# Performance work log

Hardware: AMD Instinct MI355X
Metric: run time of the kernel (lower is better)

Reference implementation:

```python
import jax, jax.numpy as jnp
import numpy as np

N_ITER = 3


def squash(v):
    # v: [..., out_C]; scale by ||v||^2/(1+||v||^2) and normalize by ||v||
    sq = jnp.sum(v * v, axis=-1, keepdims=True)
    return (sq / (1.0 + sq)) * v / jnp.sqrt(sq)


def setup_inputs() -> dict:
    key = jax.random.key(0)
    k1, k2 = jax.random.split(key)
    B, n_nodes, n_caps, in_C, out_C = 64, 2048, 32, 16, 32
    x = jax.random.normal(k1, (B, n_nodes, in_C), dtype=jnp.float32)
    route_weights = 0.1 * jax.random.normal(k2, (n_nodes, n_caps, in_C, out_C), dtype=jnp.float32)
    return {"x": x, "route_weights": route_weights}


def reference(x, route_weights):
    # priors: [B, n_nodes, n_caps, out_C]
    priors = jnp.einsum('bni,nkio->bnko', x, route_weights)
    logits = jnp.zeros_like(priors)
    outputs = None
    for i in range(N_ITER):
        probs = jax.nn.softmax(logits, axis=2)            # over n_caps
        s = jnp.sum(probs * priors, axis=1, keepdims=True)  # [B,1,n_caps,out_C]
        outputs = squash(s)
        if i != N_ITER - 1:
            delta = jnp.sum(priors * outputs, axis=-1, keepdims=True)
            logits = logits + delta
    return outputs
```

## Files before the change

### kernel.cpp

```cpp
#include <hip/hip_runtime.h>
#include <math.h>


#define BATCH 64
#define NN    2048
#define NK    32
#define NI    16
#define NO    32

#define PNB   16
#define NSETS (NN / PNB)
#define NCH   4
#define XT_JS 528

typedef __bf16 bf16x8 __attribute__((ext_vector_type(8)));
typedef float  f32x16 __attribute__((ext_vector_type(16)));

__device__ __forceinline__ unsigned short f2bf(float f) {
    unsigned int x = __float_as_uint(f);
    unsigned int lsb = (x >> 16) & 1u;
    x += 0x7fffu + lsb;
    return (unsigned short)(x >> 16);
}
__device__ __forceinline__ float bflo(unsigned int u) { return __uint_as_float(u << 16); }
__device__ __forceinline__ float bfhi(unsigned int u) { return __uint_as_float(u & 0xffff0000u); }

__global__ __launch_bounds__(256) void wqt_kernel(const float* __restrict__ Wg,
                                                  unsigned short* __restrict__ wq) {
    const int w    = threadIdx.x >> 6;
    const int lane = threadIdx.x & 63;
    const int task = blockIdx.x * 4 + w;
    const int o  = lane & 31;
    const int ih = lane >> 5;
    const float* src = Wg + (size_t)task * (NI * NO);
    unsigned short d[8];
#pragma unroll
    for (int j = 0; j < 8; ++j)
        d[j] = f2bf(src[(ih * 8 + j) * NO + o]);
    *(uint4*)(wq + (size_t)task * (NO * NI) + o * NI + ih * 8) = *(uint4*)d;
}

template <int PASS>
__global__ __launch_bounds__(1024) void fused_pass(
    const float* __restrict__ xg,
    const unsigned short* __restrict__ wq,
    const float* __restrict__ vpart,
    float* __restrict__ logits0,
    float* __restrict__ part)
{
    __shared__ unsigned short xt_lds[PNB * XT_JS];
    __shared__ float delta_lds[2][32 * 33];

    const int tid  = threadIdx.x;
    const int w    = tid >> 6;
    const int lane = tid & 63;
    const int l5   = lane & 31;
    const int h5   = lane >> 5;
    const int set  = blockIdx.x;
    const int hb   = blockIdx.y;
    const int k0   = 2 * w, k1 = 2 * w + 1;
    const int gb5  = hb * 32 + l5;
    const int sb   = tid >> 5;
    const int sk   = tid & 31;
    const int nbase = set * PNB;

#pragma unroll
    for (int rr = 0; rr < 2; ++rr) {
        const int id  = tid + rr * 1024;
        const int bl  = id >> 6;
        const int rem = id & 63;
        const int j   = rem >> 2;
        const int i4  = rem & 3;
        float4 v = *(const float4*)(xg + ((size_t)(hb * 32 + bl) * NN + (nbase + j)) * NI + i4 * 4);
        ushort4 o4;
        o4.x = f2bf(v.x); o4.y = f2bf(v.y); o4.z = f2bf(v.z); o4.w = f2bf(v.w);
        *(ushort4*)(xt_lds + j * XT_JS + bl * 16 + i4 * 4) = o4;
    }
    __syncthreads();

    unsigned orp0[8], orp1[8];
    if constexpr (PASS >= 1) {
        float v0[16], v1[16];
        float sq0 = 0.f, sq1 = 0.f;
#pragma unroll
        for (int r = 0; r < 16; ++r) {
            const int o = (r & 3) + 8 * (r >> 2) + 4 * h5;
            float a = 0.f, b = 0.f;
#pragma unroll
            for (int c = 0; c < NCH; ++c) {
                a += vpart[(((size_t)c * NK + k0) * NO + o) * BATCH + gb5];
                b += vpart[(((size_t)c * NK + k1) * NO + o) * BATCH + gb5];
            }
            v0[r] = a; v1[r] = b;
            sq0 = fmaf(a, a, sq0);
            sq1 = fmaf(b, b, sq1);
        }
        sq0 += __shfl_xor(sq0, 32);
        sq1 += __shfl_xor(sq1, 32);
        const float cf0 = sq0 / ((1.f + sq0) * sqrtf(sq0));
        const float cf1 = sq1 / ((1.f + sq1) * sqrtf(sq1));
#pragma unroll
        for (int q = 0; q < 8; ++q) {
            orp0[q] = (unsigned)f2bf(v0[2 * q] * cf0) | ((unsigned)f2bf(v0[2 * q + 1] * cf0) << 16);
            orp1[q] = (unsigned)f2bf(v1[2 * q] * cf1) | ((unsigned)f2bf(v1[2 * q + 1] * cf1) << 16);
        }
    }

    float sa0[16], sa1[16];
#pragma unroll
    for (int r = 0; r < 16; ++r) { sa0[r] = 0.f; sa1[r] = 0.f; }

    bf16x8 b0N, b1N;
    float gN = 0.f;
    {
        const int n = nbase;
        b0N = *(const bf16x8*)(wq + (size_t)n * (NK * NO * NI) + k0 * (NO * NI) + l5 * NI + h5 * 8);
        b1N = *(const bf16x8*)(wq + (size_t)n * (NK * NO * NI) + k1 * (NO * NI) + l5 * NI + h5 * 8);
        if constexpr (PASS == 2)
            gN = logits0[(size_t)n * (BATCH * NK) + hb * 1024 + tid];
    }

    int buf = 0;
    for (int j = 0; j < PNB; ++j) {
        const int n = nbase + j;
        const bf16x8 b0C = b0N, b1C = b1N;
        const float gC = gN;
        if (j < PNB - 1) {
            const int n2 = n + 1;
            b0N = *(const bf16x8*)(wq + (size_t)n2 * (NK * NO * NI) + k0 * (NO * NI) + l5 * NI + h5 * 8);
            b1N = *(const bf16x8*)(wq + (size_t)n2 * (NK * NO * NI) + k1 * (NO * NI) + l5 * NI + h5 * 8);
            if constexpr (PASS == 2)
                gN = logits0[(size_t)n2 * (BATCH * NK) + hb * 1024 + tid];
        }
        const bf16x8 aC = *(const bf16x8*)(xt_lds + j * XT_JS + l5 * 16 + h5 * 8);

        f32x16 c0, c1;
#pragma unroll
        for (int r = 0; r < 16; ++r) { c0[r] = 0.f; c1[r] = 0.f; }
        c0 = __builtin_amdgcn_mfma_f32_32x32x16_bf16(b0C, aC, c0, 0, 0, 0);
        c1 = __builtin_amdgcn_mfma_f32_32x32x16_bf16(b1C, aC, c1, 0, 0, 0);

        if constexpr (PASS == 0) {
#pragma unroll
            for (int r = 0; r < 16; ++r) { sa0[r] += c0[r]; sa1[r] += c1[r]; }
        } else {
            float d0 = 0.f, d1 = 0.f;
#pragma unroll
            for (int r = 0; r < 16; ++r) {
                const unsigned u0 = orp0[r >> 1], u1 = orp1[r >> 1];
                const float o0 = (r & 1) ? bfhi(u0) : bflo(u0);
                const float o1 = (r & 1) ? bfhi(u1) : bflo(u1);
                d0 = fmaf(c0[r], o0, d0);
                d1 = fmaf(c1[r], o1, d1);
            }
            d0 += __shfl_xor(d0, 32);
            d1 += __shfl_xor(d1, 32);

            delta_lds[buf][l5 * 33 + (h5 ? k1 : k0)] = h5 ? d1 : d0;
            __syncthreads();

            float l = delta_lds[buf][sb * 33 + sk];
            if constexpr (PASS == 1)
                logits0[(size_t)n * (BATCH * NK) + hb * 1024 + tid] = l;
            else
                l += gC;
            float e = __expf(l);
            float s = e;
#pragma unroll
            for (int mask = 1; mask < 32; mask <<= 1)
                s += __shfl_xor(s, mask);
            delta_lds[buf][sb * 33 + sk] = e / s;
            __syncthreads();

            const float p0 = delta_lds[buf][l5 * 33 + k0];
            const float p1 = delta_lds[buf][l5 * 33 + k1];
#pragma unroll
            for (int r = 0; r < 16; ++r) {
                sa0[r] = fmaf(p0, c0[r], sa0[r]);
                sa1[r] = fmaf(p1, c1[r], sa1[r]);
            }
            buf ^= 1;
        }
    }

    const float scale = (PASS == 0) ? (1.f / NK) : 1.f;
    float* pb = part + ((size_t)(hb * NSETS + set) << 15);
#pragma unroll
    for (int r = 0; r < 16; ++r) {
        const int o = (r & 3) + 8 * (r >> 2) + 4 * h5;
        pb[(k0 * NO + o) * 32 + l5] = sa0[r] * scale;
        pb[(k1 * NO + o) * 32 + l5] = sa1[r] * scale;
    }
}

__global__ __launch_bounds__(1024) void reduce_stageA(
    const float* __restrict__ part,
    float* __restrict__ vpart)
{
    const int k  = blockIdx.x;
    const int hb = blockIdx.y;
    const int c  = blockIdx.z;
    const int t  = threadIdx.x;
    const int o  = t >> 5;
    const int b  = t & 31;

    const float* src = part + ((size_t)(hb * NSETS + c * (NSETS / NCH)) << 15)
                            + (k << 10) + (o << 5) + b;
    float v0 = 0.f, v1 = 0.f, v2 = 0.f, v3 = 0.f;
#pragma unroll 4
    for (int s = 0; s < NSETS / NCH; s += 4) {
        v0 += src[(size_t)(s + 0) << 15];
        v1 += src[(size_t)(s + 1) << 15];
        v2 += src[(size_t)(s + 2) << 15];
        v3 += src[(size_t)(s + 3) << 15];
    }
    vpart[(((size_t)c * NK + k) * NO + o) * BATCH + hb * 32 + b] = (v0 + v1) + (v2 + v3);
}

__global__ __launch_bounds__(1024) void reduce_final(
    const float* __restrict__ vpart,
    float* __restrict__ outp)
{
    __shared__ float s_lds[32 * 33];
    __shared__ float cf_lds[32];
    const int k  = blockIdx.x;
    const int hb = blockIdx.y;
    const int t  = threadIdx.x;
    const int o  = t >> 5;
    const int b  = t & 31;

    float v = 0.f;
#pragma unroll
    for (int c = 0; c < NCH; ++c)
        v += vpart[(((size_t)c * NK + k) * NO + o) * BATCH + hb * 32 + b];
    s_lds[o * 33 + b] = v;
    __syncthreads();
    if (t < 32) {
        float sq = 0.f;
#pragma unroll
        for (int oo = 0; oo < 32; ++oo) { const float x = s_lds[oo * 33 + t]; sq = fmaf(x, x, sq); }
        cf_lds[t] = sq / ((1.f + sq) * sqrtf(sq));
    }
    __syncthreads();
    const int bq = t >> 5, oq = t & 31;
    outp[(size_t)(hb * 32 + bq) * 1024 + k * 32 + oq] = s_lds[oq * 33 + bq] * cf_lds[bq];
}


#define LBB 32
#define LNCHUNK 8
#define LNBLK (NN / LNCHUNK)
#define LTHREADS 512
#define WK_STRIDE 516

template <int PASS>
__global__ __launch_bounds__(LTHREADS, 1) void legacy_pass(
    const float* __restrict__ xg, const float* __restrict__ Wg,
    const float* __restrict__ outvL, float* __restrict__ logits,
    float* __restrict__ partial)
{
    __shared__ float w_lds[NK * WK_STRIDE];
    __shared__ float x_lds[LBB][NI + 1];
    __shared__ float delta_lds[LBB][NK + 1];
    const int t = threadIdx.x, nb = blockIdx.x, bg = blockIdx.y;
    const int b0 = bg * LBB;
    const int k = t >> 4, bq = t & 15, bl0 = bq * 2, bl1 = bq * 2 + 1;
    float acc0[NO], acc1[NO];
#pragma unroll
    for (int o = 0; o < NO; ++o) { acc0[o] = 0.f; acc1[o] = 0.f; }
    float outr0[NO], outr1[NO];
    if constexpr (PASS >= 1) {
        const float4* o0 = (const float4*)&outvL[((b0 + bl0) * NK + k) * NO];
        const float4* o1 = (const float4*)&outvL[((b0 + bl1) * NK + k) * NO];
#pragma unroll
        for (int q = 0; q < NO / 4; ++q) {
            float4 a = o0[q]; float4 b = o1[q];
            outr0[4*q+0]=a.x; outr0[4*q+1]=a.y; outr0[4*q+2]=a.z; outr0[4*q+3]=a.w;
            outr1[4*q+0]=b.x; outr1[4*q+1]=b.y; outr1[4*q+2]=b.z; outr1[4*q+3]=b.w;
        }
    }
    for (int j = 0; j < LNCHUNK; ++j) {
        const int n = nb * LNCHUNK + j;
        __syncthreads();
        {
            const float4* src = (const float4*)(Wg + (size_t)n * (NK * NI * NO));
#pragma unroll
            for (int r = 0; r < (NK * NI * NO / 4) / LTHREADS; ++r) {
                int idx4 = t + r * LTHREADS;
                float4 v = src[idx4];
                int e = idx4 * 4, kk = e >> 9, rem = e & 511;
                *(float4*)&w_lds[kk * WK_STRIDE + rem] = v;
            }
        }
        { int bl = t >> 4, i = t & 15;
          x_lds[bl][i] = xg[((size_t)(b0 + bl) * NN + n) * NI + i]; }
        __syncthreads();
        if constexpr (PASS == 0) {
#pragma unroll
            for (int i = 0; i < NI; ++i) {
                float xa = x_lds[bl0][i], xb = x_lds[bl1][i];
                const float* wrow = &w_lds[k * WK_STRIDE + i * NO];
#pragma unroll
                for (int o = 0; o < NO; ++o) {
                    float w = wrow[o];
                    acc0[o] = fmaf(xa, w, acc0[o]);
                    acc1[o] = fmaf(xb, w, acc1[o]);
                }
            }
        } else {
            float pr0[NO], pr1[NO];
#pragma unroll
            for (int o = 0; o < NO; ++o) { pr0[o] = 0.f; pr1[o] = 0.f; }
#pragma unroll
            for (int i = 0; i < NI; ++i) {
                float xa = x_lds[bl0][i], xb = x_lds[bl1][i];
                const float* wrow = &w_lds[k * WK_STRIDE + i * NO];
#pragma unroll
                for (int o = 0; o < NO; ++o) {
                    float w = wrow[o];
                    pr0[o] = fmaf(xa, w, pr0[o]);
                    pr1[o] = fmaf(xb, w, pr1[o]);
                }
            }
            float d0 = 0.f, d1 = 0.f;
#pragma unroll
            for (int o = 0; o < NO; ++o) {
                d0 = fmaf(pr0[o], outr0[o], d0);
                d1 = fmaf(pr1[o], outr1[o], d1);
            }
            float l0 = d0, l1 = d1;
            const size_t li0 = ((size_t)(b0 + bl0) * NN + n) * NK + k;
            const size_t li1 = ((size_t)(b0 + bl1) * NN + n) * NK + k;
            if constexpr (PASS == 2) { l0 += logits[li0]; l1 += logits[li1]; }
            else { logits[li0] = d0; logits[li1] = d1; }
            delta_lds[bl0][k] = l0; delta_lds[bl1][k] = l1;
            __syncthreads();
            float m0 = -1e30f, m1 = -1e30f;
#pragma unroll
            for (int kk = 0; kk < NK; ++kk) {
                m0 = fmaxf(m0, delta_lds[bl0][kk]);
                m1 = fmaxf(m1, delta_lds[bl1][kk]);
            }
            float s0 = 0.f, s1 = 0.f;
#pragma unroll
            for (int kk = 0; kk < NK; ++kk) {
                s0 += __expf(delta_lds[bl0][kk] - m0);
                s1 += __expf(delta_lds[bl1][kk] - m1);
            }
            float p0 = __expf(l0 - m0) / s0;
            float p1 = __expf(l1 - m1) / s1;
#pragma unroll
            for (int o = 0; o < NO; ++o) {
                acc0[o] = fmaf(p0, pr0[o], acc0[o]);
                acc1[o] = fmaf(p1, pr1[o], acc1[o]);
            }
        }
    }
    const float scale = (PASS == 0) ? (1.f / NK) : 1.f;
    float4* p0 = (float4*)&partial[(((size_t)nb * BATCH + (b0 + bl0)) * NK + k) * NO];
    float4* p1 = (float4*)&partial[(((size_t)nb * BATCH + (b0 + bl1)) * NK + k) * NO];
#pragma unroll
    for (int q = 0; q < NO / 4; ++q) {
        float4 v0, v1;
        v0.x = acc0[4*q+0]*scale; v0.y = acc0[4*q+1]*scale;
        v0.z = acc0[4*q+2]*scale; v0.w = acc0[4*q+3]*scale;
        v1.x = acc1[4*q+0]*scale; v1.y = acc1[4*q+1]*scale;
        v1.z = acc1[4*q+2]*scale; v1.w = acc1[4*q+3]*scale;
        p0[q] = v0; p1[q] = v1;
    }
}

__global__ __launch_bounds__(256) void legacy_reduce(
    const float* __restrict__ partial, float* __restrict__ outf)
{
    const int tid = blockIdx.x * 256 + threadIdx.x;
    float v = 0.f;
    for (int nb = 0; nb < LNBLK; ++nb)
        v += partial[(size_t)nb * (BATCH * NK * NO) + tid];
    float sq = v * v;
#pragma unroll
    for (int off = 1; off < 32; off <<= 1) sq += __shfl_xor(sq, off);
    float coef = sq / ((1.f + sq) * sqrtf(sq));
    outf[tid] = v * coef;
}


extern "C" void kernel_launch(void* const* d_in, const int* in_sizes, int n_in,
                              void* d_out, int out_size, void* d_ws, size_t ws_size,
                              hipStream_t stream)
{
    const float* xg = (const float*)d_in[0];
    const float* Wg = (const float*)d_in[1];
    float* outp = (float*)d_out;
    char* ws = (char*)d_ws;

    const size_t SZ_WQ     = (size_t)NN * NK * NO * NI * 2;
    const size_t SZ_PART   = (size_t)256 * 32768 * 4;
    const size_t SZ_LOGITS = (size_t)NN * BATCH * NK * 4;
    const size_t SZ_VPART  = (size_t)NCH * NK * NO * BATCH * 4;
    const size_t NEED = SZ_WQ + SZ_PART + SZ_LOGITS + SZ_VPART;

    if (ws_size >= NEED) {
        unsigned short* wq = (unsigned short*)ws;
        float* part    = (float*)(ws + SZ_WQ);
        float* logits0 = (float*)(ws + SZ_WQ + SZ_PART);
        float* vpart   = (float*)(ws + SZ_WQ + SZ_PART + SZ_LOGITS);

        wqt_kernel<<<16384, 256, 0, stream>>>(Wg, wq);

        dim3 pg(NSETS, 2);
        dim3 ra(NK, 2, NCH);
        dim3 fg(NK, 2);
        fused_pass<0><<<pg, 1024, 0, stream>>>(xg, wq, nullptr, nullptr, part);
        reduce_stageA<<<ra, 1024, 0, stream>>>(part, vpart);
        fused_pass<1><<<pg, 1024, 0, stream>>>(xg, wq, vpart, logits0, part);
        reduce_stageA<<<ra, 1024, 0, stream>>>(part, vpart);
        fused_pass<2><<<pg, 1024, 0, stream>>>(xg, wq, vpart, logits0, part);
        reduce_stageA<<<ra, 1024, 0, stream>>>(part, vpart);
        reduce_final<<<fg, 1024, 0, stream>>>(vpart, outp);
    } else {
        float* partial = (float*)ws;
        float* logits = (float*)(ws + (size_t)LNBLK * BATCH * NK * NO * 4);
        float* outvL = (float*)(ws + (size_t)LNBLK * BATCH * NK * NO * 4 + (size_t)BATCH * NN * NK * 4);
        dim3 grid(LNBLK, BATCH / LBB);
        const int rblocks = BATCH * NK * NO / 256;
        legacy_pass<0><<<grid, LTHREADS, 0, stream>>>(xg, Wg, nullptr, logits, partial);
        legacy_reduce<<<rblocks, 256, 0, stream>>>(partial, outvL);
        legacy_pass<1><<<grid, LTHREADS, 0, stream>>>(xg, Wg, outvL, logits, partial);
        legacy_reduce<<<rblocks, 256, 0, stream>>>(partial, outvL);
        legacy_pass<2><<<grid, LTHREADS, 0, stream>>>(xg, Wg, outvL, logits, partial);
        legacy_reduce<<<rblocks, 256, 0, stream>>>(partial, outp);
    }
}
```

Measured before the change: 321.6 us.

## Fuse weight bf16 conversion into first routing pass with k-split grid

```diff
diff --git a/kernel.cpp b/kernel.cpp
--- a/kernel.cpp
+++ b/kernel.cpp
@@ -12,6 +12,7 @@
 #define NSETS (NN / PNB)
 #define NCH   4
 #define XT_JS 528
+#define XT0_JS 1040
 
 typedef __bf16 bf16x8 __attribute__((ext_vector_type(8)));
 typedef float  f32x16 __attribute__((ext_vector_type(16)));
@@ -25,19 +26,71 @@
 __device__ __forceinline__ float bflo(unsigned int u) { return __uint_as_float(u << 16); }
 __device__ __forceinline__ float bfhi(unsigned int u) { return __uint_as_float(u & 0xffff0000u); }
 
-__global__ __launch_bounds__(256) void wqt_kernel(const float* __restrict__ Wg,
-                                                  unsigned short* __restrict__ wq) {
-    const int w    = threadIdx.x >> 6;
-    const int lane = threadIdx.x & 63;
-    const int task = blockIdx.x * 4 + w;
-    const int o  = lane & 31;
-    const int ih = lane >> 5;
-    const float* src = Wg + (size_t)task * (NI * NO);
-    unsigned short d[8];
-#pragma unroll
-    for (int j = 0; j < 8; ++j)
-        d[j] = f2bf(src[(ih * 8 + j) * NO + o]);
-    *(uint4*)(wq + (size_t)task * (NO * NI) + o * NI + ih * 8) = *(uint4*)d;
+__global__ __launch_bounds__(1024) void pass0_fused(
+    const float* __restrict__ xg,
+    const float* __restrict__ Wg,
+    unsigned short* __restrict__ wq,
+    float* __restrict__ part)
+{
+    __shared__ unsigned short xt_lds[PNB * XT0_JS];
+
+    const int tid   = threadIdx.x;
+    const int w     = tid >> 6;
+    const int lane  = tid & 63;
+    const int l5    = lane & 31;
+    const int h5    = lane >> 5;
+    const int set   = blockIdx.x;
+    const int khalf = blockIdx.y;
+    const int k     = khalf * 16 + w;
+    const int nbase = set * PNB;
+
+#pragma unroll
+    for (int rr = 0; rr < 4; ++rr) {
+        const int id  = tid + rr * 1024;
+        const int bl  = id >> 6;
+        const int rem = id & 63;
+        const int j   = rem >> 2;
+        const int i4  = rem & 3;
+        float4 v = *(const float4*)(xg + ((size_t)bl * NN + (nbase + j)) * NI + i4 * 4);
+        ushort4 o4;
+        o4.x = f2bf(v.x); o4.y = f2bf(v.y); o4.z = f2bf(v.z); o4.w = f2bf(v.w);
+        *(ushort4*)(xt_lds + j * XT0_JS + bl * 16 + i4 * 4) = o4;
+    }
+    __syncthreads();
+
+    float sa0[16], sa1[16];
+#pragma unroll
+    for (int r = 0; r < 16; ++r) { sa0[r] = 0.f; sa1[r] = 0.f; }
+
+    for (int j = 0; j < PNB; ++j) {
+        const int n = nbase + j;
+        const float* wsrc = Wg + ((size_t)n * NK + k) * (NI * NO) + h5 * 8 * NO + l5;
+        unsigned short us[8];
+#pragma unroll
+        for (int jj = 0; jj < 8; ++jj)
+            us[jj] = f2bf(wsrc[jj * NO]);
+        *(uint4*)(wq + ((size_t)n * NK + k) * (NO * NI) + l5 * NI + h5 * 8) = *(uint4*)us;
+        const bf16x8 bC = *(const bf16x8*)us;
+
+        const bf16x8 aA = *(const bf16x8*)(xt_lds + j * XT0_JS + l5 * 16 + h5 * 8);
+        const bf16x8 aB = *(const bf16x8*)(xt_lds + j * XT0_JS + 512 + l5 * 16 + h5 * 8);
+
+        f32x16 c0, c1;
+#pragma unroll
+        for (int r = 0; r < 16; ++r) { c0[r] = 0.f; c1[r] = 0.f; }
+        c0 = __builtin_amdgcn_mfma_f32_32x32x16_bf16(bC, aA, c0, 0, 0, 0);
+        c1 = __builtin_amdgcn_mfma_f32_32x32x16_bf16(bC, aB, c1, 0, 0, 0);
+#pragma unroll
+        for (int r = 0; r < 16; ++r) { sa0[r] += c0[r]; sa1[r] += c1[r]; }
+    }
+
+    float* pb = part + ((size_t)(khalf * NSETS + set) << 15);
+#pragma unroll
+    for (int r = 0; r < 16; ++r) {
+        const int o = (r & 3) + 8 * (r >> 2) + 4 * h5;
+        pb[(w * NO + o) * 64 + l5]      = sa0[r] * (1.f / NK);
+        pb[(w * NO + o) * 64 + 32 + l5] = sa1[r] * (1.f / NK);
+    }
 }
 
 template <int PASS>
@@ -79,7 +132,7 @@
     __syncthreads();
 
     unsigned orp0[8], orp1[8];
-    if constexpr (PASS >= 1) {
+    {
         float v0[16], v1[16];
         float sq0 = 0.f, sq1 = 0.f;
 #pragma unroll
@@ -140,56 +193,50 @@
         c0 = __builtin_amdgcn_mfma_f32_32x32x16_bf16(b0C, aC, c0, 0, 0, 0);
         c1 = __builtin_amdgcn_mfma_f32_32x32x16_bf16(b1C, aC, c1, 0, 0, 0);
 
-        if constexpr (PASS == 0) {
-#pragma unroll
-            for (int r = 0; r < 16; ++r) { sa0[r] += c0[r]; sa1[r] += c1[r]; }
-        } else {
-            float d0 = 0.f, d1 = 0.f;
-#pragma unroll
-            for (int r = 0; r < 16; ++r) {
-                const unsigned u0 = orp0[r >> 1], u1 = orp1[r >> 1];
-                const float o0 = (r & 1) ? bfhi(u0) : bflo(u0);
-                const float o1 = (r & 1) ? bfhi(u1) : bflo(u1);
-                d0 = fmaf(c0[r], o0, d0);
-                d1 = fmaf(c1[r], o1, d1);
-            }
-            d0 += __shfl_xor(d0, 32);
-            d1 += __shfl_xor(d1, 32);
-
-            delta_lds[buf][l5 * 33 + (h5 ? k1 : k0)] = h5 ? d1 : d0;
-            __syncthreads();
-
-            float l = delta_lds[buf][sb * 33 + sk];
-            if constexpr (PASS == 1)
-                logits0[(size_t)n * (BATCH * NK) + hb * 1024 + tid] = l;
-            else
-                l += gC;
-            float e = __expf(l);
-            float s = e;
-#pragma unroll
-            for (int mask = 1; mask < 32; mask <<= 1)
-                s += __shfl_xor(s, mask);
-            delta_lds[buf][sb * 33 + sk] = e / s;
-            __syncthreads();
-
-            const float p0 = delta_lds[buf][l5 * 33 + k0];
-            const float p1 = delta_lds[buf][l5 * 33 + k1];
-#pragma unroll
-            for (int r = 0; r < 16; ++r) {
-                sa0[r] = fmaf(p0, c0[r], sa0[r]);
-                sa1[r] = fmaf(p1, c1[r], sa1[r]);
-            }
-            buf ^= 1;
-        }
-    }
-
-    const float scale = (PASS == 0) ? (1.f / NK) : 1.f;
+        float d0 = 0.f, d1 = 0.f;
+#pragma unroll
+        for (int r = 0; r < 16; ++r) {
+            const unsigned u0 = orp0[r >> 1], u1 = orp1[r >> 1];
+            const float o0 = (r & 1) ? bfhi(u0) : bflo(u0);
+            const float o1 = (r & 1) ? bfhi(u1) : bflo(u1);
+            d0 = fmaf(c0[r], o0, d0);
+            d1 = fmaf(c1[r], o1, d1);
+        }
+        d0 += __shfl_xor(d0, 32);
+        d1 += __shfl_xor(d1, 32);
+
+        delta_lds[buf][l5 * 33 + (h5 ? k1 : k0)] = h5 ? d1 : d0;
+        __syncthreads();
+
+        float l = delta_lds[buf][sb * 33 + sk];
+        if constexpr (PASS == 1)
+            logits0[(size_t)n * (BATCH * NK) + hb * 1024 + tid] = l;
+        else
+            l += gC;
+        float e = __expf(l);
+        float s = e;
+#pragma unroll
+        for (int mask = 1; mask < 32; mask <<= 1)
+            s += __shfl_xor(s, mask);
+        delta_lds[buf][sb * 33 + sk] = e / s;
+        __syncthreads();
+
+        const float p0 = delta_lds[buf][l5 * 33 + k0];
+        const float p1 = delta_lds[buf][l5 * 33 + k1];
+#pragma unroll
+        for (int r = 0; r < 16; ++r) {
+            sa0[r] = fmaf(p0, c0[r], sa0[r]);
+            sa1[r] = fmaf(p1, c1[r], sa1[r]);
+        }
+        buf ^= 1;
+    }
+
     float* pb = part + ((size_t)(hb * NSETS + set) << 15);
 #pragma unroll
     for (int r = 0; r < 16; ++r) {
         const int o = (r & 3) + 8 * (r >> 2) + 4 * h5;
-        pb[(k0 * NO + o) * 32 + l5] = sa0[r] * scale;
-        pb[(k1 * NO + o) * 32 + l5] = sa1[r] * scale;
+        pb[(k0 * NO + o) * 32 + l5] = sa0[r];
+        pb[(k1 * NO + o) * 32 + l5] = sa1[r];
     }
 }
 
@@ -217,6 +264,31 @@
     vpart[(((size_t)c * NK + k) * NO + o) * BATCH + hb * 32 + b] = (v0 + v1) + (v2 + v3);
 }
 
+__global__ __launch_bounds__(1024) void reduce_stageA0(
+    const float* __restrict__ part,
+    float* __restrict__ vpart)
+{
+    const int k  = blockIdx.x;
+    const int hb = blockIdx.y;
+    const int c  = blockIdx.z;
+    const int t  = threadIdx.x;
+    const int o  = t >> 5;
+    const int b  = t & 31;
+    const int khalf = k >> 4, kk = k & 15;
+
+    const float* src = part + ((size_t)(khalf * NSETS + c * (NSETS / NCH)) << 15)
+                            + ((kk * NO + o) << 6) + hb * 32 + b;
+    float v0 = 0.f, v1 = 0.f, v2 = 0.f, v3 = 0.f;
+#pragma unroll 4
+    for (int s = 0; s < NSETS / NCH; s += 4) {
+        v0 += src[(size_t)(s + 0) << 15];
+        v1 += src[(size_t)(s + 1) << 15];
+        v2 += src[(size_t)(s + 2) << 15];
+        v3 += src[(size_t)(s + 3) << 15];
+    }
+    vpart[(((size_t)c * NK + k) * NO + o) * BATCH + hb * 32 + b] = (v0 + v1) + (v2 + v3);
+}
+
 __global__ __launch_bounds__(1024) void reduce_final(
     const float* __restrict__ vpart,
     float* __restrict__ outp)
@@ -406,13 +478,11 @@
         float* logits0 = (float*)(ws + SZ_WQ + SZ_PART);
         float* vpart   = (float*)(ws + SZ_WQ + SZ_PART + SZ_LOGITS);
 
-        wqt_kernel<<<16384, 256, 0, stream>>>(Wg, wq);
-
         dim3 pg(NSETS, 2);
         dim3 ra(NK, 2, NCH);
         dim3 fg(NK, 2);
-        fused_pass<0><<<pg, 1024, 0, stream>>>(xg, wq, nullptr, nullptr, part);
-        reduce_stageA<<<ra, 1024, 0, stream>>>(part, vpart);
+        pass0_fused<<<pg, 1024, 0, stream>>>(xg, Wg, wq, part);
+        reduce_stageA0<<<ra, 1024, 0, stream>>>(part, vpart);
         fused_pass<1><<<pg, 1024, 0, stream>>>(xg, wq, vpart, logits0, part);
         reduce_stageA<<<ra, 1024, 0, stream>>>(part, vpart);
         fused_pass<2><<<pg, 1024, 0, stream>>>(xg, wq, vpart, logits0, part);
```

After: 322.1 us. About the same (+0.2%).
